# Kernel optimization log

Measured on AMD Instinct MI355X. Metric: run time of the kernel, lower is better.

## Reference

```python
import jax, jax.numpy as jnp
import numpy as np

B = 1024      # molecules in batch
M = 128       # atoms per molecule
K = 32        # max_num_neighbors
CUTOFF = 5.0  # radius cutoff


def setup_inputs() -> dict:
    key = jax.random.key(0)
    pos = jax.random.normal(key, (B * M, 3), dtype=jnp.float32) * 3.0
    batch = (jnp.arange(B * M, dtype=jnp.int32) // M).astype(jnp.int32)
    return {"pos": pos, "batch": batch}


def reference(pos, batch):
    # pos: [N,3]; batch is sorted with M atoms per molecule -> reshape [B,M,3]
    p = pos.reshape(B, M, 3)
    sq = jnp.sum(p * p, axis=-1)  # [B,M]
    # per-molecule pairwise squared distances, [B,M,M]
    d2 = sq[:, :, None] + sq[:, None, :] - 2.0 * jnp.einsum('bic,bjc->bij', p, p)
    d2 = jnp.maximum(d2, 0.0)
    valid = d2 < CUTOFF * CUTOFF  # loop=True: self (d2=0) is included
    d2m = jnp.where(valid, d2, jnp.inf)
    neg, idx = jax.lax.top_k(-d2m, K)       # K nearest in-radius, idx: [B,M,K]
    taken = jnp.isfinite(neg)                # which slots are real edges
    local_i = jnp.arange(M, dtype=idx.dtype)
    idx = jnp.where(taken, idx, local_i[None, :, None])  # pad with self index

    # gather neighbor positions: [B,M,K,3]
    p_nb = p[jnp.arange(B)[:, None, None], idx]
    vec = p_nb - p[:, :, None, :]            # pos[edge0] - pos[edge1] (source - target)

    nonself = idx != local_i[None, :, None]
    mask = taken & nonself                   # self-loops & padding get weight 0
    sqv = jnp.sum(vec * vec, axis=-1)
    weight = jnp.where(mask, jnp.sqrt(jnp.where(mask, sqv, 1.0)), 0.0)

    node_base = (jnp.arange(B, dtype=jnp.int32) * M)[:, None, None]
    src = (node_base + idx.astype(jnp.int32)).reshape(-1)                 # edge_index[0] = neighbor j
    dst = jnp.broadcast_to(node_base + local_i.astype(jnp.int32)[None, :, None], (B, M, K)).reshape(-1)
    edge_index = jnp.stack([src, dst], axis=0)          # [2, B*M*K]
    edge_weight = weight.reshape(-1)                    # [B*M*K]
    edge_vec = vec.reshape(-1, 3)                       # [B*M*K, 3]
    return edge_index, edge_weight, edge_vec
```

## Files before the change

kernel.cpp:

```cpp
#include <hip/hip_runtime.h>
#include <stdint.h>

#define BB 1024
#define MM 128
#define KK 32
#define NEDGE (BB * MM * KK)
#define BPB 4
#define ROWS_PER_WAVE (MM / (4 * BPB))
#define HALF (ROWS_PER_WAVE / 2)

typedef unsigned int uint2v __attribute__((ext_vector_type(2)));

#define CEXS(K, ST, MSK)                                                      \
  { unsigned p_ = (unsigned)__builtin_amdgcn_ds_swizzle((int)(K), ((ST) << 10) | 0x1F); \
    unsigned mn_ = __builtin_elementwise_min((K), p_);                        \
    unsigned mx_ = __builtin_elementwise_max((K), p_);                        \
    asm("v_cndmask_b32 %0, %1, %2, %3" : "=v"(K) : "v"(mx_), "v"(mn_), "s"(MSK)); }

static __device__ __forceinline__ unsigned minxor32(unsigned k) {
#if __has_builtin(__builtin_amdgcn_permlane32_swap)
    uint2v s = __builtin_amdgcn_permlane32_swap(k, k, false, false);
    return __builtin_elementwise_min(s.x, s.y);
#else
    unsigned p = (unsigned)__shfl_xor((int)k, 32, 64);
    return __builtin_elementwise_min(k, p);
#endif
}

__global__ __launch_bounds__(256, 4) void knn_edges_kernel(const float* __restrict__ pos,
                                                           float* __restrict__ out) {
    __shared__ float px[MM], py[MM], pz[MM], sqs[MM];
    const int blk = blockIdx.x;
    const int b = blk >> 2;
    const int sub = blk & (BPB - 1);
    const int tid = threadIdx.x;

    if (tid < MM) {
        const float* p = pos + (size_t)(b * MM + tid) * 3;
        float x = p[0], y = p[1], z = p[2];
        px[tid] = x; py[tid] = y; pz[tid] = z;
        sqs[tid] = __fadd_rn(__fadd_rn(__fmul_rn(x, x), __fmul_rn(y, y)), __fmul_rn(z, z));
    }
    __syncthreads();

    const int wave = tid >> 6;
    const int lane = tid & 63;
    const int g = lane & 31;
    const bool hi = lane >= 32;
    const unsigned upper = hi ? ~0u : 0u;

    unsigned long long m1  = 0x5555555555555555ull;
    unsigned long long m2  = 0x3333333333333333ull;
    unsigned long long m4  = 0x0F0F0F0F0F0F0F0Full;
    unsigned long long m8  = 0x00FF00FF00FF00FFull;
    unsigned long long m16 = 0x0000FFFF0000FFFFull;
    asm("" : "+s"(m1), "+s"(m2), "+s"(m4), "+s"(m8), "+s"(m16));

    auto dmask = [&](int s) -> unsigned {
        unsigned zer = ((g & s) == 0) ? ~0u : 0u;
        return ~(zer ^ upper);
    };
    const unsigned f2    = dmask(2);
    const unsigned nf2   = ~f2;
    const unsigned f4c   = dmask(4);
    const unsigned f8c   = dmask(8);
    const unsigned f16c  = dmask(16);
    const unsigned f32c  = dmask(32);
    const unsigned t24   = f2 ^ f4c;
    const unsigned t48   = f4c ^ f8c;
    const unsigned t816  = f8c ^ f16c;
    const unsigned t1632 = f16c ^ f32c;
    const unsigned nf32  = ~f32c;

    const int j0 = lane, j1 = lane + 64;
    const float xa = px[j0], ya = py[j0], za = pz[j0], qa = sqs[j0];
    const float xb = px[j1], yb = py[j1], zb = pz[j1], qb = sqs[j1];

    const int row0 = sub * (MM / BPB) + wave * ROWS_PER_WAVE;
    const float fbase = (float)(b * MM);

    float* const vecbase = out + 3 * (size_t)NEDGE;
    const long e0 = (long)(b * MM + row0) * KK + g;
    float* pA = hi ? out + (size_t)NEDGE + e0 : out + e0;
    float* pB = vecbase + e0 * 3 + (hi ? 2 : 0);
    float* pC = hi ? out + 2 * (size_t)NEDGE + e0 : vecbase + e0 * 3 + 1;
    const int sC = hi ? KK : 3 * KK;
    const int oC = sC * HALF;

    for (int ii = 0; ii < HALF; ++ii) {
        const int ia = row0 + ii;
        const int ib = ia + HALF;

        const float xia = px[ia], yia = py[ia], zia = pz[ia], qia = sqs[ia];
        const float xib = px[ib], yib = py[ib], zib = pz[ib], qib = sqs[ib];

        float dot;
        dot = fmaf(xia, xa, fmaf(yia, ya, zia * za));
        unsigned K0a = ((__float_as_uint(fmaxf(fmaf(-2.0f, dot, qia + qa), 0.0f)) & 0xFFFFFF80u) | (unsigned)j0) ^ f2;
        dot = fmaf(xia, xb, fmaf(yia, yb, zia * zb));
        unsigned K1a = ((__float_as_uint(fmaxf(fmaf(-2.0f, dot, qia + qb), 0.0f)) & 0xFFFFFF80u) | (unsigned)j1) ^ nf2;
        dot = fmaf(xib, xa, fmaf(yib, ya, zib * za));
        unsigned K0b = ((__float_as_uint(fmaxf(fmaf(-2.0f, dot, qib + qa), 0.0f)) & 0xFFFFFF80u) | (unsigned)j0) ^ f2;
        dot = fmaf(xib, xb, fmaf(yib, yb, zib * zb));
        unsigned K1b = ((__float_as_uint(fmaxf(fmaf(-2.0f, dot, qib + qb), 0.0f)) & 0xFFFFFF80u) | (unsigned)j1) ^ nf2;

#define ST4(ST, MSK) CEXS(K0a, ST, MSK) CEXS(K1a, ST, MSK) CEXS(K0b, ST, MSK) CEXS(K1b, ST, MSK)
#define XOR4(V) K0a ^= (V); K1a ^= (V); K0b ^= (V); K1b ^= (V);

        ST4(1, m1)
        XOR4(t24)
        ST4(2, m2) ST4(1, m1)
        XOR4(t48)
        ST4(4, m4) ST4(2, m2) ST4(1, m1)
        XOR4(t816)
        ST4(8, m8) ST4(4, m4) ST4(2, m2) ST4(1, m1)
        XOR4(t1632)
        ST4(16, m16) ST4(8, m8) ST4(4, m4) ST4(2, m2) ST4(1, m1)
#undef ST4
#undef XOR4

        unsigned Ca = (__builtin_elementwise_min(K0a ^ f32c, K1a ^ nf32)) ^ upper;
        unsigned Cb = (__builtin_elementwise_min(K0b ^ f32c, K1b ^ nf32)) ^ upper;

#define CS2(ST, MSK) CEXS(Ca, ST, MSK) CEXS(Cb, ST, MSK)
        CS2(16, m16) CS2(8, m8) CS2(4, m4) CS2(2, m2) CS2(1, m1)
#undef CS2

        unsigned Ma = minxor32(Ca ^ upper);
        unsigned Mb = minxor32(Cb ^ upper);
#define MS2(ST, MSK) CEXS(Ma, ST, MSK) CEXS(Mb, ST, MSK)
        MS2(16, m16) MS2(8, m8) MS2(4, m4) MS2(2, m2) MS2(1, m1)
#undef MS2

        {
            const bool taken = Ma < 0x41C80000u;
            const int j = (int)(Ma & 127u);
            const int sel = taken ? j : ia;
            float dxv = __fsub_rn(px[sel], xia);
            float dyv = __fsub_rn(py[sel], yia);
            float dzv = __fsub_rn(pz[sel], zia);
            float w = sqrtf(fmaf(dzv, dzv, fmaf(dyv, dyv, dxv * dxv)));
            const float fsrc = fbase + (float)sel;
            const float fnode = fbase + (float)ia;
            pA[0] = hi ? fnode : fsrc;
            pB[0] = hi ? dzv : dxv;
            pC[0] = hi ? w : dyv;
        }
        {
            const bool taken = Mb < 0x41C80000u;
            const int j = (int)(Mb & 127u);
            const int sel = taken ? j : ib;
            float dxv = __fsub_rn(px[sel], xib);
            float dyv = __fsub_rn(py[sel], yib);
            float dzv = __fsub_rn(pz[sel], zib);
            float w = sqrtf(fmaf(dzv, dzv, fmaf(dyv, dyv, dxv * dxv)));
            const float fsrc = fbase + (float)sel;
            const float fnode = fbase + (float)ib;
            pA[HALF * KK] = hi ? fnode : fsrc;
            pB[HALF * 3 * KK] = hi ? dzv : dxv;
            pC[oC] = hi ? w : dyv;
        }
        pA += KK; pB += 3 * KK; pC += sC;
    }
}

extern "C" void kernel_launch(void* const* d_in, const int* in_sizes, int n_in,
                              void* d_out, int out_size, void* d_ws, size_t ws_size,
                              hipStream_t stream) {
    const float* pos = (const float*)d_in[0];
    float* out = (float*)d_out;
    hipLaunchKernelGGL(knn_edges_kernel, dim3(BB * BPB), dim3(256), 0, stream, pos, out);
}
```

Measured before the change: 46.50 us.

## Compact in-radius candidates via ballot and sort 64 with DPP bitonic network

Result: faster. 39.68 us (-14.7%).

```diff
diff --git a/kernel.cpp b/kernel.cpp
--- a/kernel.cpp
+++ b/kernel.cpp
@@ -7,15 +7,53 @@
 #define NEDGE (BB * MM * KK)
 #define BPB 4
 #define ROWS_PER_WAVE (MM / (4 * BPB))
-#define HALF (ROWS_PER_WAVE / 2)
+
+#define TH 0x41C80000u
+#define INFK 0x7F800000u
 
 typedef unsigned int uint2v __attribute__((ext_vector_type(2)));
 
-#define CEXS(K, ST, MSK)                                                      \
-  { unsigned p_ = (unsigned)__builtin_amdgcn_ds_swizzle((int)(K), ((ST) << 10) | 0x1F); \
-    unsigned mn_ = __builtin_elementwise_min((K), p_);                        \
-    unsigned mx_ = __builtin_elementwise_max((K), p_);                        \
-    asm("v_cndmask_b32 %0, %1, %2, %3" : "=v"(K) : "v"(mx_), "v"(mn_), "s"(MSK)); }
+#define DPP1 "quad_perm:[1,0,3,2] row_mask:0xf bank_mask:0xf"
+#define DPP2 "quad_perm:[2,3,0,1] row_mask:0xf bank_mask:0xf"
+
+template<int ST>
+static __device__ __forceinline__ void cexd(unsigned& k, unsigned long long msk) {
+    unsigned t0, t1;
+    if constexpr (ST == 1) {
+        asm("s_nop 1\n\t"
+            "v_min_u32_dpp %1, %0, %0 " DPP1 "\n\t"
+            "v_max_u32_dpp %2, %0, %0 " DPP1 "\n\t"
+            "v_cndmask_b32 %0, %2, %1, %3"
+            : "+v"(k), "=&v"(t0), "=&v"(t1) : "s"(msk));
+    } else {
+        asm("s_nop 1\n\t"
+            "v_min_u32_dpp %1, %0, %0 " DPP2 "\n\t"
+            "v_max_u32_dpp %2, %0, %0 " DPP2 "\n\t"
+            "v_cndmask_b32 %0, %2, %1, %3"
+            : "+v"(k), "=&v"(t0), "=&v"(t1) : "s"(msk));
+    }
+}
+
+template<int ST>
+static __device__ __forceinline__ void cexs(unsigned& k, unsigned long long msk) {
+    unsigned p = (unsigned)__builtin_amdgcn_ds_swizzle((int)k, (ST << 10) | 0x1F);
+    unsigned mn = __builtin_elementwise_min(k, p);
+    unsigned mx = __builtin_elementwise_max(k, p);
+    asm("v_cndmask_b32 %0, %1, %2, %3" : "=v"(k) : "v"(mx), "v"(mn), "s"(msk));
+}
+
+static __device__ __forceinline__ void cex32f(unsigned& k, unsigned long long msk) {
+#if __has_builtin(__builtin_amdgcn_permlane32_swap)
+    uint2v s = __builtin_amdgcn_permlane32_swap(k, k, false, false);
+    unsigned mn = __builtin_elementwise_min(s.x, s.y);
+    unsigned mx = __builtin_elementwise_max(s.x, s.y);
+#else
+    unsigned p = (unsigned)__shfl_xor((int)k, 32, 64);
+    unsigned mn = __builtin_elementwise_min(k, p);
+    unsigned mx = __builtin_elementwise_max(k, p);
+#endif
+    asm("v_cndmask_b32 %0, %1, %2, %3" : "=v"(k) : "v"(mx), "v"(mn), "s"(msk));
+}
 
 static __device__ __forceinline__ unsigned minxor32(unsigned k) {
 #if __has_builtin(__builtin_amdgcn_permlane32_swap)
@@ -27,9 +65,15 @@
 #endif
 }
 
+static __device__ __forceinline__ unsigned mbcnt64(unsigned long long m) {
+    unsigned t = __builtin_amdgcn_mbcnt_lo((unsigned)m, 0u);
+    return __builtin_amdgcn_mbcnt_hi((unsigned)(m >> 32), t);
+}
+
 __global__ __launch_bounds__(256, 4) void knn_edges_kernel(const float* __restrict__ pos,
                                                            float* __restrict__ out) {
     __shared__ float px[MM], py[MM], pz[MM], sqs[MM];
+    __shared__ unsigned comp[4][64];
     const int blk = blockIdx.x;
     const int b = blk >> 2;
     const int sub = blk & (BPB - 1);
@@ -54,7 +98,8 @@
     unsigned long long m4  = 0x0F0F0F0F0F0F0F0Full;
     unsigned long long m8  = 0x00FF00FF00FF00FFull;
     unsigned long long m16 = 0x0000FFFF0000FFFFull;
-    asm("" : "+s"(m1), "+s"(m2), "+s"(m4), "+s"(m8), "+s"(m16));
+    unsigned long long m32 = 0x00000000FFFFFFFFull;
+    asm("" : "+s"(m1), "+s"(m2), "+s"(m4), "+s"(m8), "+s"(m16), "+s"(m32));
 
     auto dmask = [&](int s) -> unsigned {
         unsigned zer = ((g & s) == 0) ? ~0u : 0u;
@@ -72,6 +117,14 @@
     const unsigned t1632 = f16c ^ f32c;
     const unsigned nf32  = ~f32c;
 
+    auto ff = [&](int s) -> unsigned { return (lane & s) ? ~0u : 0u; };
+    const unsigned u2    = ff(2);
+    const unsigned s24   = u2 ^ ff(4);
+    const unsigned s48   = ff(4) ^ ff(8);
+    const unsigned s816  = ff(8) ^ ff(16);
+    const unsigned s1632 = ff(16) ^ ff(32);
+    const unsigned u32   = ff(32);
+
     const int j0 = lane, j1 = lane + 64;
     const float xa = px[j0], ya = py[j0], za = pz[j0], qa = sqs[j0];
     const float xb = px[j1], yb = py[j1], zb = pz[j1], qb = sqs[j1];
@@ -85,82 +138,94 @@
     float* pB = vecbase + e0 * 3 + (hi ? 2 : 0);
     float* pC = hi ? out + 2 * (size_t)NEDGE + e0 : vecbase + e0 * 3 + 1;
     const int sC = hi ? KK : 3 * KK;
-    const int oC = sC * HALF;
-
-    for (int ii = 0; ii < HALF; ++ii) {
-        const int ia = row0 + ii;
-        const int ib = ia + HALF;
-
-        const float xia = px[ia], yia = py[ia], zia = pz[ia], qia = sqs[ia];
-        const float xib = px[ib], yib = py[ib], zib = pz[ib], qib = sqs[ib];
-
-        float dot;
-        dot = fmaf(xia, xa, fmaf(yia, ya, zia * za));
-        unsigned K0a = ((__float_as_uint(fmaxf(fmaf(-2.0f, dot, qia + qa), 0.0f)) & 0xFFFFFF80u) | (unsigned)j0) ^ f2;
-        dot = fmaf(xia, xb, fmaf(yia, yb, zia * zb));
-        unsigned K1a = ((__float_as_uint(fmaxf(fmaf(-2.0f, dot, qia + qb), 0.0f)) & 0xFFFFFF80u) | (unsigned)j1) ^ nf2;
-        dot = fmaf(xib, xa, fmaf(yib, ya, zib * za));
-        unsigned K0b = ((__float_as_uint(fmaxf(fmaf(-2.0f, dot, qib + qa), 0.0f)) & 0xFFFFFF80u) | (unsigned)j0) ^ f2;
-        dot = fmaf(xib, xb, fmaf(yib, yb, zib * zb));
-        unsigned K1b = ((__float_as_uint(fmaxf(fmaf(-2.0f, dot, qib + qb), 0.0f)) & 0xFFFFFF80u) | (unsigned)j1) ^ nf2;
-
-#define ST4(ST, MSK) CEXS(K0a, ST, MSK) CEXS(K1a, ST, MSK) CEXS(K0b, ST, MSK) CEXS(K1b, ST, MSK)
-#define XOR4(V) K0a ^= (V); K1a ^= (V); K0b ^= (V); K1b ^= (V);
-
-        ST4(1, m1)
-        XOR4(t24)
-        ST4(2, m2) ST4(1, m1)
-        XOR4(t48)
-        ST4(4, m4) ST4(2, m2) ST4(1, m1)
-        XOR4(t816)
-        ST4(8, m8) ST4(4, m4) ST4(2, m2) ST4(1, m1)
-        XOR4(t1632)
-        ST4(16, m16) ST4(8, m8) ST4(4, m4) ST4(2, m2) ST4(1, m1)
-#undef ST4
-#undef XOR4
-
-        unsigned Ca = (__builtin_elementwise_min(K0a ^ f32c, K1a ^ nf32)) ^ upper;
-        unsigned Cb = (__builtin_elementwise_min(K0b ^ f32c, K1b ^ nf32)) ^ upper;
-
-#define CS2(ST, MSK) CEXS(Ca, ST, MSK) CEXS(Cb, ST, MSK)
-        CS2(16, m16) CS2(8, m8) CS2(4, m4) CS2(2, m2) CS2(1, m1)
-#undef CS2
-
-        unsigned Ma = minxor32(Ca ^ upper);
-        unsigned Mb = minxor32(Cb ^ upper);
-#define MS2(ST, MSK) CEXS(Ma, ST, MSK) CEXS(Mb, ST, MSK)
-        MS2(16, m16) MS2(8, m8) MS2(4, m4) MS2(2, m2) MS2(1, m1)
-#undef MS2
-
-        {
-            const bool taken = Ma < 0x41C80000u;
-            const int j = (int)(Ma & 127u);
-            const int sel = taken ? j : ia;
-            float dxv = __fsub_rn(px[sel], xia);
-            float dyv = __fsub_rn(py[sel], yia);
-            float dzv = __fsub_rn(pz[sel], zia);
-            float w = sqrtf(fmaf(dzv, dzv, fmaf(dyv, dyv, dxv * dxv)));
-            const float fsrc = fbase + (float)sel;
-            const float fnode = fbase + (float)ia;
-            pA[0] = hi ? fnode : fsrc;
-            pB[0] = hi ? dzv : dxv;
-            pC[0] = hi ? w : dyv;
+
+    float fnode = (float)(b * MM + row0);
+
+    for (int i = row0; i < row0 + ROWS_PER_WAVE; ++i) {
+        const float xi = px[i], yi = py[i], zi = pz[i], qi = sqs[i];
+
+        float dot0 = fmaf(xi, xa, fmaf(yi, ya, zi * za));
+        float d20 = fmaxf(fmaf(-2.0f, dot0, qi + qa), 0.0f);
+        unsigned k0r = (__float_as_uint(d20) & 0xFFFFFF80u) | (unsigned)j0;
+        float dot1 = fmaf(xi, xb, fmaf(yi, yb, zi * zb));
+        float d21 = fmaxf(fmaf(-2.0f, dot1, qi + qb), 0.0f);
+        unsigned k1r = (__float_as_uint(d21) & 0xFFFFFF80u) | (unsigned)j1;
+
+        unsigned long long mask0 = __ballot(k0r < TH);
+        unsigned long long mask1 = __ballot(k1r < TH);
+        unsigned c0 = (unsigned)__popcll(mask0);
+        unsigned nsurv = c0 + (unsigned)__popcll(mask1);
+
+        unsigned mdup;
+        if (nsurv <= 64u) {
+            unsigned dest0 = mbcnt64(mask0);
+            unsigned dest1 = c0 + mbcnt64(mask1);
+            if (k0r < TH) comp[wave][dest0] = k0r;
+            if (k1r < TH) comp[wave][dest1] = k1r;
+            asm volatile("s_waitcnt lgkmcnt(0)" ::: "memory");
+            unsigned k = comp[wave][lane];
+            k = ((unsigned)lane < nsurv) ? k : INFK;
+
+            k ^= u2;
+            cexd<1>(k, m1);
+            k ^= s24;
+            cexd<2>(k, m2); cexd<1>(k, m1);
+            k ^= s48;
+            cexs<4>(k, m4); cexd<2>(k, m2); cexd<1>(k, m1);
+            k ^= s816;
+            cexs<8>(k, m8); cexs<4>(k, m4); cexd<2>(k, m2); cexd<1>(k, m1);
+            k ^= s1632;
+            cexs<16>(k, m16); cexs<8>(k, m8); cexs<4>(k, m4);
+            cexd<2>(k, m2); cexd<1>(k, m1);
+            k ^= u32;
+            cex32f(k, m32); cexs<16>(k, m16); cexs<8>(k, m8); cexs<4>(k, m4);
+            cexd<2>(k, m2); cexd<1>(k, m1);
+
+#if __has_builtin(__builtin_amdgcn_permlane32_swap)
+            uint2v s = __builtin_amdgcn_permlane32_swap(k, k, false, false);
+            unsigned partner = s.x ^ s.y ^ k;
+#else
+            unsigned partner = (unsigned)__shfl_xor((int)k, 32, 64);
+#endif
+            asm("v_cndmask_b32 %0, %1, %2, %3" : "=v"(mdup) : "v"(partner), "v"(k), "s"(m32));
+        } else {
+            unsigned K0 = k0r ^ f2;
+            unsigned K1 = k1r ^ nf2;
+#define SS2(ST, MSK) cexs<ST>(K0, MSK); cexs<ST>(K1, MSK);
+            SS2(1, m1)
+            K0 ^= t24; K1 ^= t24;
+            SS2(2, m2) SS2(1, m1)
+            K0 ^= t48; K1 ^= t48;
+            SS2(4, m4) SS2(2, m2) SS2(1, m1)
+            K0 ^= t816; K1 ^= t816;
+            SS2(8, m8) SS2(4, m4) SS2(2, m2) SS2(1, m1)
+            K0 ^= t1632; K1 ^= t1632;
+            SS2(16, m16) SS2(8, m8) SS2(4, m4) SS2(2, m2) SS2(1, m1)
+#undef SS2
+            unsigned Ca = (__builtin_elementwise_min(K0 ^ f32c, K1 ^ nf32)) ^ upper;
+            cexs<16>(Ca, m16); cexs<8>(Ca, m8); cexs<4>(Ca, m4);
+            cexs<2>(Ca, m2);  cexs<1>(Ca, m1);
+            unsigned Ma = minxor32(Ca ^ upper);
+            cexs<16>(Ma, m16); cexs<8>(Ma, m8); cexs<4>(Ma, m4);
+            cexs<2>(Ma, m2);  cexs<1>(Ma, m1);
+            mdup = Ma;
         }
-        {
-            const bool taken = Mb < 0x41C80000u;
-            const int j = (int)(Mb & 127u);
-            const int sel = taken ? j : ib;
-            float dxv = __fsub_rn(px[sel], xib);
-            float dyv = __fsub_rn(py[sel], yib);
-            float dzv = __fsub_rn(pz[sel], zib);
-            float w = sqrtf(fmaf(dzv, dzv, fmaf(dyv, dyv, dxv * dxv)));
-            const float fsrc = fbase + (float)sel;
-            const float fnode = fbase + (float)ib;
-            pA[HALF * KK] = hi ? fnode : fsrc;
-            pB[HALF * 3 * KK] = hi ? dzv : dxv;
-            pC[oC] = hi ? w : dyv;
-        }
+
+        const bool taken = mdup < TH;
+        const int j = (int)(mdup & 127u);
+        const int sel = taken ? j : i;
+
+        float dxv = __fsub_rn(px[sel], xi);
+        float dyv = __fsub_rn(py[sel], yi);
+        float dzv = __fsub_rn(pz[sel], zi);
+        float w = sqrtf(fmaf(dzv, dzv, fmaf(dyv, dyv, dxv * dxv)));
+        const float fsrc = fbase + (float)sel;
+
+        pA[0] = hi ? fnode : fsrc;
+        pB[0] = hi ? dzv : dxv;
+        pC[0] = hi ? w : dyv;
         pA += KK; pB += 3 * KK; pC += sC;
+        fnode += 1.0f;
     }
 }
 
```
